# Kernel tuning notes

Hardware: AMD Instinct MI355X
Metric: run time of the kernel (lower is better)

The kernel has to match this reference:

```python
import jax, jax.numpy as jnp
import numpy as np
import math

NUM_HEADS = 16
EMBED = 1024
B, S = 128, 512


def setup_inputs() -> dict:
    key = jax.random.key(0)
    ks = jax.random.split(key, 9)
    scale = 1.0 / math.sqrt(EMBED)
    return {
        "queries": jax.random.normal(ks[0], (B, S, EMBED), dtype=jnp.float32),
        "keys": jax.random.normal(ks[1], (B, S, EMBED), dtype=jnp.float32),
        "values": jax.random.normal(ks[2], (B, S, EMBED), dtype=jnp.float32),
        "Wq": jax.random.normal(ks[3], (EMBED, EMBED), dtype=jnp.float32) * scale,
        "bq": jax.random.normal(ks[4], (EMBED,), dtype=jnp.float32) * scale,
        "Wk": jax.random.normal(ks[5], (EMBED, EMBED), dtype=jnp.float32) * scale,
        "bk": jax.random.normal(ks[6], (EMBED,), dtype=jnp.float32) * scale,
        "Wv": jax.random.normal(ks[7], (EMBED, EMBED), dtype=jnp.float32) * scale,
        "bv": jax.random.normal(ks[8], (EMBED,), dtype=jnp.float32) * scale,
    }


def reference(queries, keys, values, Wq, bq, Wk, bk, Wv, bv):
    H = NUM_HEADS
    E = queries.shape[-1]
    d = E // H
    # torch nn.Linear: y = x @ W.T + b
    q = queries @ Wq.T + bq  # [B, S, E]
    k = keys @ Wk.T + bk
    v = values @ Wv.T + bv
    n_q = q.shape[1]
    n_k = k.shape[1]
    n_v = v.shape[1]
    # Faithful to the original: reshape with seq-len as the LEADING dim,
    # which reinterprets the (B, S, E) buffer as (S, B, H, d).
    q = q.reshape(n_q, -1, H, d)  # [S, B, H, d]
    k = k.reshape(n_k, -1, H, d)
    # attention over the second (batch-like) axis; scores: [S, H, B, B]
    scores = jnp.einsum('nqhd,nkhd->nhqk', q, k) / math.sqrt(d)
    attn = jax.nn.softmax(scores, axis=-1)
    v = v.reshape(n_v, -1, H, d)  # [S, B, H, d]
    out = jnp.einsum('nhql,nlhd->nqhd', attn, v)  # [S, B, H, d]
    n_a = out.shape[0]
    return out.reshape(-1, n_a, H * d)  # [B, S, E]
```

## Files before the change

### kernel.cpp

```cpp
#include <hip/hip_runtime.h>
#include <hip/hip_bf16.h>

typedef unsigned short u16;
typedef __attribute__((ext_vector_type(8))) short bf16x8;
typedef __attribute__((ext_vector_type(4))) float f32x4;
typedef __attribute__((ext_vector_type(4))) float vfloat4;
typedef __attribute__((ext_vector_type(4))) unsigned short ushort4v;
typedef __attribute__((ext_vector_type(8))) unsigned short ushort8v;

#define DEV __device__ __forceinline__
#define AS1 __attribute__((address_space(1)))
#define AS3 __attribute__((address_space(3)))

#define BARRIER()  __builtin_amdgcn_s_barrier()
#define LGKM0()    asm volatile("s_waitcnt lgkmcnt(0)" ::: "memory")
#define VMCNT0()   asm volatile("s_waitcnt vmcnt(0)" ::: "memory")
#define VMCNT4()   asm volatile("s_waitcnt vmcnt(4)" ::: "memory")
#define SCHED0()   __builtin_amdgcn_sched_barrier(0)

DEV u16 f2bf(float f) {
    union { float f; unsigned u; } v; v.f = f;
    unsigned r = v.u + 0x7FFFu + ((v.u >> 16) & 1u);
    return (u16)(r >> 16);
}

DEV void gload_lds16(const void* g, void* l) {
    __builtin_amdgcn_global_load_lds((const AS1 unsigned int*)g,
                                     (AS3 unsigned int*)l, 16, 0, 0);
}

static constexpr int KDIM = 1024;
static constexpr int NROW = 65536;

__global__ __launch_bounds__(256)
void cvt_f32_bf16(const float* __restrict__ src, u16* __restrict__ dst, unsigned n8)
{
    unsigned stride = gridDim.x * blockDim.x;
    for (unsigned i = blockIdx.x * blockDim.x + threadIdx.x; i < n8; i += stride) {
        size_t base = (size_t)i * 8;
        vfloat4 a = *(const vfloat4*)(src + base);
        vfloat4 b = *(const vfloat4*)(src + base + 4);
        ushort8v o;
#pragma unroll
        for (int j = 0; j < 4; ++j) { o[j] = f2bf(a[j]); o[j + 4] = f2bf(b[j]); }
        *(ushort8v*)(dst + base) = o;
    }
}

__global__ __launch_bounds__(512)
__attribute__((amdgpu_waves_per_eu(1, 2)))
void proj_gemm_8ph(const u16* __restrict__ X, const u16* __restrict__ W,
                   const float* __restrict__ bias, u16* __restrict__ Y)
{
    __shared__ __align__(16) u16 As[2][256 * 64];
    __shared__ __align__(16) u16 Bs[2][256 * 64];

    int bx = blockIdx.x;
    int wg = (bx & 7) * 128 + (bx >> 3);
    int bm = wg >> 2;
    int bn = wg & 3;

    int tid  = threadIdx.x;
    int lane = tid & 63;
    int wid  = tid >> 6;
    int wm   = wid >> 2;
    int wn   = wid & 3;
    int l15  = lane & 15;
    int l4   = lane >> 4;

    const u16* Xp = X + (size_t)bm * 256 * KDIM;
    const u16* Wp = W + (size_t)bn * 256 * KDIM;

    int srow_in = tid >> 3;
    int scol16  = (tid & 7) ^ (srow_in & 7);

    f32x4 acc[8][4] = {};

#define STAGE(lds, gbase, slot, h, kt)                                           \
    {                                                                            \
        const u16* src_ = (gbase) + (size_t)((h) * 128 + srow_in) * KDIM         \
                          + (kt) * 64 + scol16 * 8;                              \
        gload_lds16(src_, &lds[slot][((h) * 128 + wid * 8) * 64]);               \
        gload_lds16(src_ + (size_t)64 * KDIM,                                    \
                    &lds[slot][((h) * 128 + 64 + wid * 8) * 64]);                \
    }

#define READ_AF(slot, mh)                                                        \
    {                                                                            \
        _Pragma("unroll")                                                        \
        for (int mi = 0; mi < 4; ++mi) {                                         \
            int row = wm * 128 + (mh) * 64 + mi * 16 + l15;                      \
            unsigned o0 = (unsigned)(row * 128 + l4 * 16) ^ (unsigned)((row & 7) << 4); \
            af[mi][0] = *(const bf16x8*)((const char*)As[slot] + o0);            \
            af[mi][1] = *(const bf16x8*)((const char*)As[slot] + (o0 ^ 64u));    \
        }                                                                        \
    }

#define READ_BF(dst, slot, nh)                                                   \
    {                                                                            \
        _Pragma("unroll")                                                        \
        for (int ni = 0; ni < 2; ++ni) {                                         \
            int row = wn * 64 + (nh) * 32 + ni * 16 + l15;                       \
            unsigned o0 = (unsigned)(row * 128 + l4 * 16) ^ (unsigned)((row & 7) << 4); \
            dst[ni][0] = *(const bf16x8*)((const char*)Bs[slot] + o0);           \
            dst[ni][1] = *(const bf16x8*)((const char*)Bs[slot] + (o0 ^ 64u));   \
        }                                                                        \
    }

#define MFMA_Q(mlo, bb, nlo)                                                     \
    __builtin_amdgcn_s_setprio(1);                                               \
    _Pragma("unroll")                                                            \
    for (int kk = 0; kk < 2; ++kk) {                                             \
        _Pragma("unroll")                                                        \
        for (int mi = 0; mi < 4; ++mi) {                                         \
            _Pragma("unroll")                                                    \
            for (int ni = 0; ni < 2; ++ni)                                       \
                acc[(mlo) + mi][(nlo) + ni] = __builtin_amdgcn_mfma_f32_16x16x32_bf16( \
                    af[mi][kk], bb[ni][kk], acc[(mlo) + mi][(nlo) + ni], 0, 0, 0); \
        }                                                                        \
    }                                                                            \
    __builtin_amdgcn_s_setprio(0);

    STAGE(As, Xp, 0, 0, 0);
    STAGE(As, Xp, 0, 1, 0);
    STAGE(Bs, Wp, 0, 0, 0);
    STAGE(Bs, Wp, 0, 1, 0);
    STAGE(As, Xp, 1, 0, 1);
    STAGE(As, Xp, 1, 1, 1);
    STAGE(Bs, Wp, 1, 0, 1);
    STAGE(Bs, Wp, 1, 1, 1);
    VMCNT0();
    BARRIER();

    for (int it = 0; it < 8; ++it) {
        int c12 = 2 * it + 1;
        int c36 = (2 * it + 2 < 16) ? 2 * it + 2 : 15;
        int c78 = (2 * it + 3 < 16) ? 2 * it + 3 : 15;
        bf16x8 af[4][2], b0[2][2], b1[2][2];

        READ_AF(0, 0); READ_BF(b0, 0, 0); READ_BF(b1, 0, 1);
        STAGE(As, Xp, 1, 0, c12); STAGE(As, Xp, 1, 1, c12);
        BARRIER(); LGKM0(); SCHED0();
        MFMA_Q(0, b0, 0); MFMA_Q(0, b1, 2);
        BARRIER();

        READ_AF(0, 1);
        STAGE(Bs, Wp, 0, 0, c36); STAGE(Bs, Wp, 0, 1, c36);
        VMCNT4(); BARRIER(); LGKM0(); SCHED0();
        MFMA_Q(4, b0, 0); MFMA_Q(4, b1, 2);
        BARRIER();

        READ_AF(1, 0); READ_BF(b0, 1, 0); READ_BF(b1, 1, 1);
        STAGE(As, Xp, 0, 0, c36); STAGE(As, Xp, 0, 1, c36);
        BARRIER(); LGKM0(); SCHED0();
        MFMA_Q(0, b0, 0); MFMA_Q(0, b1, 2);
        BARRIER();

        READ_AF(1, 1);
        STAGE(Bs, Wp, 1, 0, c78); STAGE(Bs, Wp, 1, 1, c78);
        VMCNT4(); BARRIER(); LGKM0(); SCHED0();
        MFMA_Q(4, b0, 0); MFMA_Q(4, b1, 2);
        BARRIER();
    }
    VMCNT0();
    BARRIER();

    u16* Cs = &As[0][0];
#pragma unroll
    for (int p = 0; p < 2; ++p) {
        if (wm == p) {
#pragma unroll
            for (int ni = 0; ni < 4; ++ni) {
                float bv = bias[bn * 256 + wn * 64 + ni * 16 + l15];
#pragma unroll
                for (int mi = 0; mi < 8; ++mi) {
                    int c2 = (wn * 64 + ni * 16 + l15) * 2;
#pragma unroll
                    for (int r = 0; r < 4; ++r) {
                        int row = mi * 16 + l4 * 4 + r;
                        unsigned off = (unsigned)(row * 512 + c2) ^ (unsigned)((row & 7) << 4);
                        *(u16*)((char*)Cs + off) = f2bf(acc[mi][ni][r] + bv);
                    }
                }
            }
        }
        __syncthreads();
#pragma unroll
        for (int i = 0; i < 8; ++i) {
            int idx = tid + i * 512;
            int row = idx >> 5;
            int c16 = idx & 31;
            unsigned off = (unsigned)(row * 512 + c16 * 16) ^ (unsigned)((row & 7) << 4);
            ushort8v v = *(const ushort8v*)((const char*)Cs + off);
            *(ushort8v*)&Y[(size_t)(bm * 256 + p * 128 + row) * KDIM
                           + bn * 256 + c16 * 8] = v;
        }
        __syncthreads();
    }
#undef STAGE
#undef READ_AF
#undef READ_BF
#undef MFMA_Q
}

__global__ __launch_bounds__(256)
void proj_gemm(const float* __restrict__ X, const float* __restrict__ W,
               const float* __restrict__ bias, u16* __restrict__ Y)
{
    __shared__ u16 As[128 * 64];
    __shared__ u16 Bs[128 * 64];

    int bx = blockIdx.x;
    int wg = (bx & 7) * 512 + (bx >> 3);
    int bm = wg >> 3;
    int bn = wg & 7;

    int tid  = threadIdx.x;
    int lane = tid & 63;
    int wid  = tid >> 6;
    int wrow = (wid >> 1) * 64;
    int wcol = (wid & 1) * 64;
    int l15 = lane & 15;
    int l4  = lane >> 4;

    int srow = tid >> 4;
    int scol = (tid & 15) * 4;

    const float* Xp = X + (size_t)bm * 128 * KDIM;
    const float* Wp = W + (size_t)bn * 128 * KDIM;

    f32x4 acc[4][4] = {};

    for (int k0 = 0; k0 < KDIM; k0 += 64) {
        __syncthreads();
#pragma unroll
        for (int r = 0; r < 8; ++r) {
            int row = r * 16 + srow;
            vfloat4 a = *(const vfloat4*)(Xp + (size_t)row * KDIM + k0 + scol);
            vfloat4 b = *(const vfloat4*)(Wp + (size_t)row * KDIM + k0 + scol);
            ushort4v ap, bp;
#pragma unroll
            for (int j = 0; j < 4; ++j) { ap[j] = f2bf(a[j]); bp[j] = f2bf(b[j]); }
            unsigned off = (unsigned)(row * 128 + scol * 2) ^ (unsigned)((row & 7) << 4);
            *(ushort4v*)((char*)As + off) = ap;
            *(ushort4v*)((char*)Bs + off) = bp;
        }
        __syncthreads();
#pragma unroll
        for (int kk = 0; kk < 2; ++kk) {
            bf16x8 af[4], bfr[4];
#pragma unroll
            for (int mi = 0; mi < 4; ++mi) {
                int row = wrow + mi * 16 + l15;
                unsigned off = (unsigned)(row * 128 + kk * 64 + l4 * 16) ^ (unsigned)((row & 7) << 4);
                af[mi] = *(const bf16x8*)((char*)As + off);
            }
#pragma unroll
            for (int ni = 0; ni < 4; ++ni) {
                int row = wcol + ni * 16 + l15;
                unsigned off = (unsigned)(row * 128 + kk * 64 + l4 * 16) ^ (unsigned)((row & 7) << 4);
                bfr[ni] = *(const bf16x8*)((char*)Bs + off);
            }
#pragma unroll
            for (int mi = 0; mi < 4; ++mi)
#pragma unroll
                for (int ni = 0; ni < 4; ++ni)
                    acc[mi][ni] = __builtin_amdgcn_mfma_f32_16x16x32_bf16(
                        af[mi], bfr[ni], acc[mi][ni], 0, 0, 0);
        }
    }

#pragma unroll
    for (int ni = 0; ni < 4; ++ni) {
        int col = bn * 128 + wcol + ni * 16 + l15;
        float bv = bias[col];
#pragma unroll
        for (int mi = 0; mi < 4; ++mi) {
            int row0 = bm * 128 + wrow + mi * 16 + l4 * 4;
#pragma unroll
            for (int r = 0; r < 4; ++r)
                Y[(size_t)(row0 + r) * KDIM + col] = f2bf(acc[mi][ni][r] + bv);
        }
    }
}

__global__ __launch_bounds__(256)
void attn_kernel(const u16* __restrict__ Qg, const u16* __restrict__ Kg,
                 const u16* __restrict__ Vg, float* __restrict__ Out)
{
    __shared__ u16 Qs[128 * 64];
    __shared__ u16 KVs[64 * 136];
    __shared__ u16 Ps[128 * 136];

    int g = blockIdx.x >> 4;
    int h = blockIdx.x & 15;

    int tid  = threadIdx.x;
    int lane = tid & 63;
    int wid  = tid >> 6;
    int l15 = lane & 15, l4 = lane >> 4;
    int qbase = wid * 32;

    size_t rowbase = (size_t)g * 128 * 1024 + (size_t)h * 64;

    {
        int r  = tid >> 1;
        int c0 = (tid & 1) * 32;
        const u16* qsrc = Qg + rowbase + (size_t)r * 1024 + c0;
        const u16* ksrc = Kg + rowbase + (size_t)r * 1024 + c0;
#pragma unroll
        for (int i = 0; i < 4; ++i) {
            ushort8v qv = *(const ushort8v*)(qsrc + i * 8);
            ushort8v kv = *(const ushort8v*)(ksrc + i * 8);
            unsigned off = (unsigned)(r * 128 + (c0 + i * 8) * 2) ^ (unsigned)((r & 7) << 4);
            *(ushort8v*)((char*)Qs + off) = qv;
            *(ushort8v*)((char*)KVs + off) = kv;
        }
    }
    __syncthreads();

    f32x4 st[8][2] = {};
#pragma unroll
    for (int kk = 0; kk < 2; ++kk) {
        bf16x8 kf[8];
#pragma unroll
        for (int mi = 0; mi < 8; ++mi) {
            int row = mi * 16 + l15;
            unsigned off = (unsigned)(row * 128 + kk * 64 + l4 * 16) ^ (unsigned)((row & 7) << 4);
            kf[mi] = *(const bf16x8*)((char*)KVs + off);
        }
#pragma unroll
        for (int qi = 0; qi < 2; ++qi) {
            int row = qbase + qi * 16 + l15;
            unsigned off = (unsigned)(row * 128 + kk * 64 + l4 * 16) ^ (unsigned)((row & 7) << 4);
            bf16x8 qf = *(const bf16x8*)((char*)Qs + off);
#pragma unroll
            for (int mi = 0; mi < 8; ++mi)
                st[mi][qi] = __builtin_amdgcn_mfma_f32_16x16x32_bf16(kf[mi], qf, st[mi][qi], 0, 0, 0);
        }
    }
    __syncthreads();

    {
        int r  = tid >> 1;
        int c0 = (tid & 1) * 32;
        const u16* vsrc = Vg + rowbase + (size_t)r * 1024 + c0;
#pragma unroll
        for (int i = 0; i < 4; ++i) {
            ushort8v vv = *(const ushort8v*)(vsrc + i * 8);
#pragma unroll
            for (int e = 0; e < 8; ++e)
                KVs[(c0 + i * 8 + e) * 136 + r] = vv[e];
        }
    }

    const float cexp = 0.125f * 1.44269504088896f;
#pragma unroll
    for (int qi = 0; qi < 2; ++qi) {
        float m = -3.0e38f;
#pragma unroll
        for (int mi = 0; mi < 8; ++mi)
#pragma unroll
            for (int r = 0; r < 4; ++r) m = fmaxf(m, st[mi][qi][r]);
        m = fmaxf(m, __shfl_xor(m, 16));
        m = fmaxf(m, __shfl_xor(m, 32));
        float s = 0.f;
#pragma unroll
        for (int mi = 0; mi < 8; ++mi)
#pragma unroll
            for (int r = 0; r < 4; ++r) {
                float p = exp2f((st[mi][qi][r] - m) * cexp);
                st[mi][qi][r] = p;
                s += p;
            }
        s += __shfl_xor(s, 16);
        s += __shfl_xor(s, 32);
        float inv = 1.0f / s;
        int q = qbase + qi * 16 + l15;
#pragma unroll
        for (int mi = 0; mi < 8; ++mi) {
            ushort4v pp;
#pragma unroll
            for (int r = 0; r < 4; ++r) pp[r] = f2bf(st[mi][qi][r] * inv);
            *(ushort4v*)((char*)Ps + (unsigned)(q * 272 + mi * 32 + l4 * 8)) = pp;
        }
    }
    __syncthreads();

    f32x4 o[2][4] = {};
#pragma unroll
    for (int kk = 0; kk < 4; ++kk) {
        bf16x8 pa[2];
#pragma unroll
        for (int mf = 0; mf < 2; ++mf) {
            int q = qbase + mf * 16 + l15;
            pa[mf] = *(const bf16x8*)((char*)Ps + (unsigned)(q * 272 + kk * 64 + l4 * 16));
        }
#pragma unroll
        for (int nf = 0; nf < 4; ++nf) {
            int d = nf * 16 + l15;
            bf16x8 vb = *(const bf16x8*)((char*)KVs + (unsigned)(d * 272 + kk * 64 + l4 * 16));
#pragma unroll
            for (int mf = 0; mf < 2; ++mf)
                o[mf][nf] = __builtin_amdgcn_mfma_f32_16x16x32_bf16(pa[mf], vb, o[mf][nf], 0, 0, 0);
        }
    }

#pragma unroll
    for (int mf = 0; mf < 2; ++mf)
#pragma unroll
        for (int nf = 0; nf < 4; ++nf) {
            int d  = nf * 16 + l15;
            int q0 = qbase + mf * 16 + l4 * 4;
#pragma unroll
            for (int r = 0; r < 4; ++r)
                Out[(size_t)(g * 128 + q0 + r) * 1024 + h * 64 + d] = o[mf][nf][r];
        }
}

extern "C" void kernel_launch(void* const* d_in, const int* in_sizes, int n_in,
                              void* d_out, int out_size, void* d_ws, size_t ws_size,
                              hipStream_t stream)
{
    const float* Xq = (const float*)d_in[0];
    const float* Xk = (const float*)d_in[1];
    const float* Xv = (const float*)d_in[2];
    const float* Wq = (const float*)d_in[3];
    const float* bq = (const float*)d_in[4];
    const float* Wk = (const float*)d_in[5];
    const float* bk = (const float*)d_in[6];
    const float* Wv = (const float*)d_in[7];
    const float* bv = (const float*)d_in[8];

    const size_t NE = (size_t)NROW * KDIM;
    const size_t WE = (size_t)KDIM * KDIM;

    u16* Qw = (u16*)d_ws;
    u16* Kw = Qw + NE;
    u16* Vw = Kw + NE;

    size_t need = NE * 2 * 3 + NE * 2 + WE * 2 * 3;

    if (ws_size >= need) {
        u16* Xb  = Vw + NE;
        u16* Wb0 = Xb + NE;
        u16* Wb1 = Wb0 + WE;
        u16* Wb2 = Wb1 + WE;

        cvt_f32_bf16<<<dim3(512),  dim3(256), 0, stream>>>(Wq, Wb0, (unsigned)(WE / 8));
        cvt_f32_bf16<<<dim3(512),  dim3(256), 0, stream>>>(Wk, Wb1, (unsigned)(WE / 8));
        cvt_f32_bf16<<<dim3(512),  dim3(256), 0, stream>>>(Wv, Wb2, (unsigned)(WE / 8));

        cvt_f32_bf16<<<dim3(2048), dim3(256), 0, stream>>>(Xq, Xb, (unsigned)(NE / 8));
        proj_gemm_8ph<<<dim3(1024), dim3(512), 0, stream>>>(Xb, Wb0, bq, Qw);
        cvt_f32_bf16<<<dim3(2048), dim3(256), 0, stream>>>(Xk, Xb, (unsigned)(NE / 8));
        proj_gemm_8ph<<<dim3(1024), dim3(512), 0, stream>>>(Xb, Wb1, bk, Kw);
        cvt_f32_bf16<<<dim3(2048), dim3(256), 0, stream>>>(Xv, Xb, (unsigned)(NE / 8));
        proj_gemm_8ph<<<dim3(1024), dim3(512), 0, stream>>>(Xb, Wb2, bv, Vw);
    } else {
        proj_gemm<<<dim3(4096), dim3(256), 0, stream>>>(Xq, Wq, bq, Qw);
        proj_gemm<<<dim3(4096), dim3(256), 0, stream>>>(Xk, Wk, bk, Kw);
        proj_gemm<<<dim3(4096), dim3(256), 0, stream>>>(Xv, Wv, bv, Vw);
    }

    attn_kernel<<<dim3(512 * 16), dim3(256), 0, stream>>>(Qw, Kw, Vw, (float*)d_out);
}
```

Baseline: 850.2 us.

## Fuse fp32-to-bf16 activation conversion into projection GEMM LDS pipeline

Removes the separate activation conversion kernels. The GEMM now stages fp32 activation tiles straight into LDS and converts them to bf16 in registers before the MFMAs. K-tile depth is halved to 32 to fit the fp32 tile, which doubles the main-loop iterations and barriers. This drops a full fp32 read plus a bf16 write and read of the activations, at the cost of in-loop conversion ALU work and more synchronisation per unit of K.

```diff
diff --git a/kernel.cpp b/kernel.cpp
--- a/kernel.cpp
+++ b/kernel.cpp
@@ -15,13 +15,20 @@
 #define BARRIER()  __builtin_amdgcn_s_barrier()
 #define LGKM0()    asm volatile("s_waitcnt lgkmcnt(0)" ::: "memory")
 #define VMCNT0()   asm volatile("s_waitcnt vmcnt(0)" ::: "memory")
-#define VMCNT4()   asm volatile("s_waitcnt vmcnt(4)" ::: "memory")
+#define VMCNT2()   asm volatile("s_waitcnt vmcnt(2)" ::: "memory")
 #define SCHED0()   __builtin_amdgcn_sched_barrier(0)
 
 DEV u16 f2bf(float f) {
     union { float f; unsigned u; } v; v.f = f;
     unsigned r = v.u + 0x7FFFu + ((v.u >> 16) & 1u);
     return (u16)(r >> 16);
+}
+
+DEV short f2bf_hw(float f) {
+    __hip_bfloat16 h = __float2bfloat16(f);
+    short s;
+    __builtin_memcpy(&s, &h, 2);
+    return s;
 }
 
 DEV void gload_lds16(const void* g, void* l) {
@@ -49,11 +56,11 @@
 
 __global__ __launch_bounds__(512)
 __attribute__((amdgpu_waves_per_eu(1, 2)))
-void proj_gemm_8ph(const u16* __restrict__ X, const u16* __restrict__ W,
+void proj_gemm_8ph(const float* __restrict__ X, const u16* __restrict__ W,
                    const float* __restrict__ bias, u16* __restrict__ Y)
 {
-    __shared__ __align__(16) u16 As[2][256 * 64];
-    __shared__ __align__(16) u16 Bs[2][256 * 64];
+    __shared__ __align__(16) float Asf[2][256 * 32];
+    __shared__ __align__(16) u16   Bs[2][256 * 32];
 
     int bx = blockIdx.x;
     int wg = (bx & 7) * 128 + (bx >> 3);
@@ -68,104 +75,125 @@
     int l15  = lane & 15;
     int l4   = lane >> 4;
 
-    const u16* Xp = X + (size_t)bm * 256 * KDIM;
-    const u16* Wp = W + (size_t)bn * 256 * KDIM;
-
-    int srow_in = tid >> 3;
-    int scol16  = (tid & 7) ^ (srow_in & 7);
+    const float* Xp = X + (size_t)bm * 256 * KDIM;
+    const u16*   Wp = W + (size_t)bn * 256 * KDIM;
+
+    int arow = tid >> 3;
+    int ags  = (tid & 7) ^ (arow & 7);
+    int brow = tid >> 2;
+    int bgs  = (tid & 3) ^ (brow & 3);
 
     f32x4 acc[8][4] = {};
 
-#define STAGE(lds, gbase, slot, h, kt)                                           \
+#define STAGE_A(slot, kt)                                                        \
     {                                                                            \
-        const u16* src_ = (gbase) + (size_t)((h) * 128 + srow_in) * KDIM         \
-                          + (kt) * 64 + scol16 * 8;                              \
-        gload_lds16(src_, &lds[slot][((h) * 128 + wid * 8) * 64]);               \
-        gload_lds16(src_ + (size_t)64 * KDIM,                                    \
-                    &lds[slot][((h) * 128 + 64 + wid * 8) * 64]);                \
-    }
-
-#define READ_AF(slot, mh)                                                        \
+        _Pragma("unroll")                                                        \
+        for (int j = 0; j < 4; ++j)                                              \
+            gload_lds16(Xp + (size_t)(j * 64 + arow) * KDIM + (kt) * 32 + ags * 4, \
+                        &Asf[slot][(j * 64 + wid * 8) * 32]);                    \
+    }
+
+#define STAGE_B(slot, kt)                                                        \
+    {                                                                            \
+        _Pragma("unroll")                                                        \
+        for (int j = 0; j < 2; ++j)                                              \
+            gload_lds16(Wp + (size_t)(j * 128 + brow) * KDIM + (kt) * 32 + bgs * 8, \
+                        &Bs[slot][(j * 128 + wid * 16) * 32]);                   \
+    }
+
+#define READ_A_LOAD(slot, mh)                                                    \
     {                                                                            \
         _Pragma("unroll")                                                        \
         for (int mi = 0; mi < 4; ++mi) {                                         \
             int row = wm * 128 + (mh) * 64 + mi * 16 + l15;                      \
-            unsigned o0 = (unsigned)(row * 128 + l4 * 16) ^ (unsigned)((row & 7) << 4); \
-            af[mi][0] = *(const bf16x8*)((const char*)As[slot] + o0);            \
-            af[mi][1] = *(const bf16x8*)((const char*)As[slot] + (o0 ^ 64u));    \
+            unsigned g0 = (unsigned)((2 * l4)     ^ (row & 7));                  \
+            unsigned g1 = (unsigned)((2 * l4 + 1) ^ (row & 7));                  \
+            ar[mi][0] = *(const f32x4*)((const char*)Asf[slot] + row * 128 + g0 * 16); \
+            ar[mi][1] = *(const f32x4*)((const char*)Asf[slot] + row * 128 + g1 * 16); \
         }                                                                        \
     }
 
-#define READ_BF(dst, slot, nh)                                                   \
+#define CVT_AF()                                                                 \
     {                                                                            \
         _Pragma("unroll")                                                        \
+        for (int mi = 0; mi < 4; ++mi) {                                         \
+            bf16x8 v;                                                            \
+            _Pragma("unroll")                                                    \
+            for (int e = 0; e < 4; ++e) {                                        \
+                v[e]     = f2bf_hw(ar[mi][0][e]);                                \
+                v[e + 4] = f2bf_hw(ar[mi][1][e]);                                \
+            }                                                                    \
+            af[mi] = v;                                                          \
+        }                                                                        \
+    }
+
+#define READ_BF(dst, slot, nlo)                                                  \
+    {                                                                            \
+        _Pragma("unroll")                                                        \
         for (int ni = 0; ni < 2; ++ni) {                                         \
-            int row = wn * 64 + (nh) * 32 + ni * 16 + l15;                       \
-            unsigned o0 = (unsigned)(row * 128 + l4 * 16) ^ (unsigned)((row & 7) << 4); \
-            dst[ni][0] = *(const bf16x8*)((const char*)Bs[slot] + o0);           \
-            dst[ni][1] = *(const bf16x8*)((const char*)Bs[slot] + (o0 ^ 64u));   \
+            int row = wn * 64 + ((nlo) + ni) * 16 + l15;                         \
+            dst[ni] = *(const bf16x8*)((const char*)Bs[slot] + row * 64          \
+                        + ((unsigned)(l4 ^ (row & 3)) << 4));                    \
         }                                                                        \
     }
 
-#define MFMA_Q(mlo, bb, nlo)                                                     \
+#define MFMA_Q8(mlo, bb, nlo)                                                    \
     __builtin_amdgcn_s_setprio(1);                                               \
     _Pragma("unroll")                                                            \
-    for (int kk = 0; kk < 2; ++kk) {                                             \
-        _Pragma("unroll")                                                        \
-        for (int mi = 0; mi < 4; ++mi) {                                         \
-            _Pragma("unroll")                                                    \
-            for (int ni = 0; ni < 2; ++ni)                                       \
-                acc[(mlo) + mi][(nlo) + ni] = __builtin_amdgcn_mfma_f32_16x16x32_bf16( \
-                    af[mi][kk], bb[ni][kk], acc[(mlo) + mi][(nlo) + ni], 0, 0, 0); \
-        }                                                                        \
+    for (int mi = 0; mi < 4; ++mi) {                                             \
+        _Pragma("unroll")                                                        \
+        for (int ni = 0; ni < 2; ++ni)                                           \
+            acc[(mlo) + mi][(nlo) + ni] = __builtin_amdgcn_mfma_f32_16x16x32_bf16( \
+                af[mi], bb[ni], acc[(mlo) + mi][(nlo) + ni], 0, 0, 0);           \
     }                                                                            \
     __builtin_amdgcn_s_setprio(0);
 
-    STAGE(As, Xp, 0, 0, 0);
-    STAGE(As, Xp, 0, 1, 0);
-    STAGE(Bs, Wp, 0, 0, 0);
-    STAGE(Bs, Wp, 0, 1, 0);
-    STAGE(As, Xp, 1, 0, 1);
-    STAGE(As, Xp, 1, 1, 1);
-    STAGE(Bs, Wp, 1, 0, 1);
-    STAGE(Bs, Wp, 1, 1, 1);
+    STAGE_A(0, 0);
+    STAGE_B(0, 0);
+    STAGE_A(1, 1);
+    STAGE_B(1, 1);
     VMCNT0();
     BARRIER();
 
-    for (int it = 0; it < 8; ++it) {
+    for (int it = 0; it < 16; ++it) {
         int c12 = 2 * it + 1;
-        int c36 = (2 * it + 2 < 16) ? 2 * it + 2 : 15;
-        int c78 = (2 * it + 3 < 16) ? 2 * it + 3 : 15;
-        bf16x8 af[4][2], b0[2][2], b1[2][2];
-
-        READ_AF(0, 0); READ_BF(b0, 0, 0); READ_BF(b1, 0, 1);
-        STAGE(As, Xp, 1, 0, c12); STAGE(As, Xp, 1, 1, c12);
+        int c36 = (2 * it + 2 < 32) ? 2 * it + 2 : 31;
+        int c78 = (2 * it + 3 < 32) ? 2 * it + 3 : 31;
+        f32x4 ar[4][2];
+        bf16x8 af[4], b0[2], b1[2];
+
+        READ_A_LOAD(0, 0); READ_BF(b0, 0, 0); READ_BF(b1, 0, 2);
+        STAGE_A(1, c12);
         BARRIER(); LGKM0(); SCHED0();
-        MFMA_Q(0, b0, 0); MFMA_Q(0, b1, 2);
+        CVT_AF();
+        MFMA_Q8(0, b0, 0); MFMA_Q8(0, b1, 2);
         BARRIER();
 
-        READ_AF(0, 1);
-        STAGE(Bs, Wp, 0, 0, c36); STAGE(Bs, Wp, 0, 1, c36);
-        VMCNT4(); BARRIER(); LGKM0(); SCHED0();
-        MFMA_Q(4, b0, 0); MFMA_Q(4, b1, 2);
+        READ_A_LOAD(0, 1);
+        STAGE_B(0, c36);
+        VMCNT2(); BARRIER(); LGKM0(); SCHED0();
+        CVT_AF();
+        MFMA_Q8(4, b0, 0); MFMA_Q8(4, b1, 2);
         BARRIER();
 
-        READ_AF(1, 0); READ_BF(b0, 1, 0); READ_BF(b1, 1, 1);
-        STAGE(As, Xp, 0, 0, c36); STAGE(As, Xp, 0, 1, c36);
+        READ_A_LOAD(1, 0); READ_BF(b0, 1, 0); READ_BF(b1, 1, 2);
+        STAGE_A(0, c36);
         BARRIER(); LGKM0(); SCHED0();
-        MFMA_Q(0, b0, 0); MFMA_Q(0, b1, 2);
+        CVT_AF();
+        MFMA_Q8(0, b0, 0); MFMA_Q8(0, b1, 2);
         BARRIER();
 
-        READ_AF(1, 1);
-        STAGE(Bs, Wp, 1, 0, c78); STAGE(Bs, Wp, 1, 1, c78);
-        VMCNT4(); BARRIER(); LGKM0(); SCHED0();
-        MFMA_Q(4, b0, 0); MFMA_Q(4, b1, 2);
+        READ_A_LOAD(1, 1);
+        STAGE_B(1, c78);
+        VMCNT2(); BARRIER(); LGKM0(); SCHED0();
+        CVT_AF();
+        MFMA_Q8(4, b0, 0); MFMA_Q8(4, b1, 2);
         BARRIER();
     }
     VMCNT0();
     BARRIER();
 
-    u16* Cs = &As[0][0];
+    u16* Cs = (u16*)&Asf[0][0];
 #pragma unroll
     for (int p = 0; p < 2; ++p) {
         if (wm == p) {
@@ -197,10 +225,12 @@
         }
         __syncthreads();
     }
-#undef STAGE
-#undef READ_AF
+#undef STAGE_A
+#undef STAGE_B
+#undef READ_A_LOAD
+#undef CVT_AF
 #undef READ_BF
-#undef MFMA_Q
+#undef MFMA_Q8
 }
 
 __global__ __launch_bounds__(256)
@@ -439,24 +469,20 @@
     u16* Kw = Qw + NE;
     u16* Vw = Kw + NE;
 
-    size_t need = NE * 2 * 3 + NE * 2 + WE * 2 * 3;
+    size_t need = NE * 2 * 3 + WE * 2 * 3;
 
     if (ws_size >= need) {
-        u16* Xb  = Vw + NE;
-        u16* Wb0 = Xb + NE;
+        u16* Wb0 = Vw + NE;
         u16* Wb1 = Wb0 + WE;
         u16* Wb2 = Wb1 + WE;
 
-        cvt_f32_bf16<<<dim3(512),  dim3(256), 0, stream>>>(Wq, Wb0, (unsigned)(WE / 8));
-        cvt_f32_bf16<<<dim3(512),  dim3(256), 0, stream>>>(Wk, Wb1, (unsigned)(WE / 8));
-        cvt_f32_bf16<<<dim3(512),  dim3(256), 0, stream>>>(Wv, Wb2, (unsigned)(WE / 8));
-
-        cvt_f32_bf16<<<dim3(2048), dim3(256), 0, stream>>>(Xq, Xb, (unsigned)(NE / 8));
-        proj_gemm_8ph<<<dim3(1024), dim3(512), 0, stream>>>(Xb, Wb0, bq, Qw);
-        cvt_f32_bf16<<<dim3(2048), dim3(256), 0, stream>>>(Xk, Xb, (unsigned)(NE / 8));
-        proj_gemm_8ph<<<dim3(1024), dim3(512), 0, stream>>>(Xb, Wb1, bk, Kw);
-        cvt_f32_bf16<<<dim3(2048), dim3(256), 0, stream>>>(Xv, Xb, (unsigned)(NE / 8));
-        proj_gemm_8ph<<<dim3(1024), dim3(512), 0, stream>>>(Xb, Wb2, bv, Vw);
+        cvt_f32_bf16<<<dim3(512), dim3(256), 0, stream>>>(Wq, Wb0, (unsigned)(WE / 8));
+        cvt_f32_bf16<<<dim3(512), dim3(256), 0, stream>>>(Wk, Wb1, (unsigned)(WE / 8));
+        cvt_f32_bf16<<<dim3(512), dim3(256), 0, stream>>>(Wv, Wb2, (unsigned)(WE / 8));
+
+        proj_gemm_8ph<<<dim3(1024), dim3(512), 0, stream>>>(Xq, Wb0, bq, Qw);
+        proj_gemm_8ph<<<dim3(1024), dim3(512), 0, stream>>>(Xk, Wb1, bk, Kw);
+        proj_gemm_8ph<<<dim3(1024), dim3(512), 0, stream>>>(Xv, Wb2, bv, Vw);
     } else {
         proj_gemm<<<dim3(4096), dim3(256), 0, stream>>>(Xq, Wq, bq, Qw);
         proj_gemm<<<dim3(4096), dim3(256), 0, stream>>>(Xk, Wk, bk, Kw);
```

Result: slower. 869.5 us (+2.3%).
